# Optimization experiments

Measured on AMD Instinct MI355X. Metric: run time of the kernel, lower is better.

## Reference

```python
import jax, jax.numpy as jnp
import numpy as np

EMB = 1024
HEADS = 16
HEAD_DIM = EMB // HEADS
EPS = 1e-5


def gelu_tanh(x):
    c = jnp.sqrt(jnp.asarray(2.0 / jnp.pi, x.dtype))
    return 0.5 * x * (1.0 + jnp.tanh(c * (x + 0.044715 * x ** 3)))


def layernorm(x, scale, shift):
    mean = jnp.mean(x, axis=-1, keepdims=True)
    var = jnp.mean((x - mean) ** 2, axis=-1, keepdims=True)
    return scale * (x - mean) / jnp.sqrt(var + EPS) + shift


def setup_inputs() -> dict:
    key = jax.random.key(0)
    ks = jax.random.split(key, 12)
    s = 0.02
    return {
        "x": jax.random.normal(ks[0], (2, 2048, EMB), dtype=jnp.float32),
        "Wq": jax.random.normal(ks[1], (EMB, EMB), dtype=jnp.float32) * s,
        "Wk": jax.random.normal(ks[2], (EMB, EMB), dtype=jnp.float32) * s,
        "Wv": jax.random.normal(ks[3], (EMB, EMB), dtype=jnp.float32) * s,
        "Wo": jax.random.normal(ks[4], (EMB, EMB), dtype=jnp.float32) * s,
        "bo": jnp.zeros((EMB,), dtype=jnp.float32),
        "W1": jax.random.normal(ks[5], (EMB, 4 * EMB), dtype=jnp.float32) * s,
        "b1": jnp.zeros((4 * EMB,), dtype=jnp.float32),
        "W2": jax.random.normal(ks[6], (4 * EMB, EMB), dtype=jnp.float32) * s,
        "b2": jnp.zeros((EMB,), dtype=jnp.float32),
        "ln1_scale": jnp.ones((EMB,), dtype=jnp.float32),
        "ln1_shift": jnp.zeros((EMB,), dtype=jnp.float32),
        "ln2_scale": jnp.ones((EMB,), dtype=jnp.float32),
        "ln2_shift": jnp.zeros((EMB,), dtype=jnp.float32),
    }


def reference(x, Wq, Wk, Wv, Wo, bo, W1, b1, W2, b2,
              ln1_scale, ln1_shift, ln2_scale, ln2_shift):
    b, n, d = x.shape
    # --- attention sublayer (pre-LN) ---
    h = layernorm(x, ln1_scale, ln1_shift)
    q = (h @ Wq).reshape(b, n, HEADS, HEAD_DIM).transpose(0, 2, 1, 3)  # [b,h,n,hd]
    k = (h @ Wk).reshape(b, n, HEADS, HEAD_DIM).transpose(0, 2, 1, 3)
    v = (h @ Wv).reshape(b, n, HEADS, HEAD_DIM).transpose(0, 2, 1, 3)
    scores = jnp.einsum('bhqd,bhkd->bhqk', q, k)  # [b,h,n,n]
    causal = jnp.tril(jnp.ones((n, n), dtype=bool))  # True = keep
    scores = jnp.where(causal, scores, -jnp.inf)
    weights = jax.nn.softmax(scores / np.sqrt(HEAD_DIM), axis=-1)
    ctx = jnp.einsum('bhqk,bhkd->bqhd', weights, v).reshape(b, n, d)
    attn_out = ctx @ Wo + bo
    x = x + attn_out
    # --- FFN sublayer (pre-LN) ---
    h = layernorm(x, ln2_scale, ln2_shift)
    h = gelu_tanh(h @ W1 + b1) @ W2 + b2
    return x + h
```

## Files before the change

kernel.cpp:

```cpp
#include <hip/hip_runtime.h>
#include <hip/hip_bf16.h>


using bf16 = __hip_bfloat16;
using bf16x8 = __attribute__((ext_vector_type(8))) short;
using f32x4 = __attribute__((ext_vector_type(4))) float;

#define MFMA16(a, b, c) __builtin_amdgcn_mfma_f32_16x16x32_bf16((a), (b), (c), 0, 0, 0)

enum { EPI_BF16 = 0, EPI_BIAS_RES_F32 = 1, EPI_GELU_BF16 = 2 };

__device__ __forceinline__ float cvt_f(float x) { return x; }
__device__ __forceinline__ float cvt_f(bf16 x) { return __bfloat162float(x); }

__device__ __forceinline__ float gelu_f(float x) {
  float z = 0.7978845608028654f * (x + 0.044715f * x * x * x);
  z = fminf(fmaxf(z, -15.f), 15.f);
  float e = __expf(2.f * z);
  return 0.5f * x * (1.f + (e - 1.f) / (e + 1.f));
}

__device__ __forceinline__ void stage16(const bf16* g, bf16* lds_base, int lane) {
#if defined(__has_builtin) && __has_builtin(__builtin_amdgcn_global_load_lds)
  __builtin_amdgcn_global_load_lds(
      (__attribute__((address_space(1))) void*)(void*)g,
      (__attribute__((address_space(3))) void*)lds_base, 16, 0, 0);
#else
  *(int4*)(lds_base + lane * 8) = *(const int4*)g;
#endif
}

template <typename T>
__global__ __launch_bounds__(256) void transpose_bf16_k(
    const T* __restrict__ src, bf16* __restrict__ dst, int sld, int dld) {
  __shared__ float tile[32][33];
  const int tx = threadIdx.x & 31, ty = threadIdx.x >> 5;
  const size_t r0 = (size_t)blockIdx.y * 32, c0 = (size_t)blockIdx.x * 32;
#pragma unroll
  for (int i = 0; i < 32; i += 8)
    tile[ty + i][tx] = cvt_f(src[(r0 + ty + i) * sld + c0 + tx]);
  __syncthreads();
#pragma unroll
  for (int i = 0; i < 32; i += 8)
    dst[(c0 + ty + i) * dld + r0 + tx] = __float2bfloat16(tile[tx][ty + i]);
}

__global__ __launch_bounds__(256) void ln_fwd_k(
    const float* __restrict__ x, const float* __restrict__ gam,
    const float* __restrict__ bet, bf16* __restrict__ out) {
  const int row = blockIdx.x;
  const float4 v = ((const float4*)(x + (size_t)row * 1024))[threadIdx.x];
  float s = v.x + v.y + v.z + v.w;
  float sq = v.x * v.x + v.y * v.y + v.z * v.z + v.w * v.w;
#pragma unroll
  for (int off = 32; off; off >>= 1) {
    s += __shfl_down(s, off);
    sq += __shfl_down(sq, off);
  }
  __shared__ float rs[4], rq[4];
  const int w = threadIdx.x >> 6, lane = threadIdx.x & 63;
  if (lane == 0) { rs[w] = s; rq[w] = sq; }
  __syncthreads();
  s = rs[0] + rs[1] + rs[2] + rs[3];
  sq = rq[0] + rq[1] + rq[2] + rq[3];
  const float mean = s * (1.f / 1024.f);
  const float var = sq * (1.f / 1024.f) - mean * mean;
  const float rstd = rsqrtf(var + 1e-5f);
  const float4 g4 = ((const float4*)gam)[threadIdx.x];
  const float4 b4 = ((const float4*)bet)[threadIdx.x];
  short4 pk;
  bf16* hp = (bf16*)&pk;
  hp[0] = __float2bfloat16((v.x - mean) * rstd * g4.x + b4.x);
  hp[1] = __float2bfloat16((v.y - mean) * rstd * g4.y + b4.y);
  hp[2] = __float2bfloat16((v.z - mean) * rstd * g4.z + b4.z);
  hp[3] = __float2bfloat16((v.w - mean) * rstd * g4.w + b4.w);
  ((short4*)(out + (size_t)row * 1024))[threadIdx.x] = pk;
}

template <int EPI>
__global__ __launch_bounds__(256) void gemm_bt_k(
    const bf16* __restrict__ A, const bf16* __restrict__ BT,
    void* __restrict__ Cout, const float* __restrict__ bias,
    const float* __restrict__ res, int M, int N, int K) {
  __shared__ bf16 As[128 * 64];
  __shared__ bf16 Bs[128 * 64];
  const int tid = threadIdx.x;
  const int w = tid >> 6, lane = tid & 63;
  const int wr = w >> 1, wc = w & 1;
  const int lr = lane & 15, lk = lane >> 4;
  const size_t rowTile = (size_t)blockIdx.y * 128;
  const size_t colTile = (size_t)blockIdx.x * 128;

  const bf16* Ag = A + rowTile * K;
  const bf16* Bg = BT + colTile * K;
  const int srow = lane >> 3;
  const int scol = (lane & 7) * 8;

  const f32x4 z4 = {0.f, 0.f, 0.f, 0.f};
  f32x4 acc[4][4];
#pragma unroll
  for (int i = 0; i < 4; ++i)
#pragma unroll
    for (int j = 0; j < 4; ++j) acc[i][j] = z4;

  for (int kb = 0; kb < K; kb += 64) {
#pragma unroll
    for (int i = 0; i < 4; ++i) {
      const int r = w * 32 + i * 8;
      stage16(Ag + (size_t)(r + srow) * K + kb + scol, &As[r * 64], lane);
      stage16(Bg + (size_t)(r + srow) * K + kb + scol, &Bs[r * 64], lane);
    }
    __syncthreads();
#pragma unroll
    for (int kk = 0; kk < 2; ++kk) {
      bf16x8 af[4], bg[4];
#pragma unroll
      for (int mi = 0; mi < 4; ++mi)
        af[mi] = *(const bf16x8*)&As[(wr * 64 + mi * 16 + lr) * 64 + kk * 32 + lk * 8];
#pragma unroll
      for (int ni = 0; ni < 4; ++ni)
        bg[ni] = *(const bf16x8*)&Bs[(wc * 64 + ni * 16 + lr) * 64 + kk * 32 + lk * 8];
#pragma unroll
      for (int mi = 0; mi < 4; ++mi)
#pragma unroll
        for (int ni = 0; ni < 4; ++ni)
          acc[mi][ni] = MFMA16(af[mi], bg[ni], acc[mi][ni]);
    }
    __syncthreads();
  }

  const size_t baseRow = rowTile + wr * 64;
  const size_t baseCol = colTile + wc * 64;
#pragma unroll
  for (int mi = 0; mi < 4; ++mi)
#pragma unroll
    for (int ni = 0; ni < 4; ++ni) {
      const size_t col = baseCol + ni * 16 + lr;
#pragma unroll
      for (int r = 0; r < 4; ++r) {
        const size_t row = baseRow + mi * 16 + lk * 4 + r;
        const size_t idx = row * (size_t)N + col;
        const float v = acc[mi][ni][r];
        if constexpr (EPI == EPI_BF16) {
          ((bf16*)Cout)[idx] = __float2bfloat16(v);
        } else if constexpr (EPI == EPI_BIAS_RES_F32) {
          ((float*)Cout)[idx] = v + bias[col] + res[idx];
        } else {
          ((bf16*)Cout)[idx] = __float2bfloat16(gelu_f(v + bias[col]));
        }
      }
    }
}

__global__ __launch_bounds__(256) void attn_fwd_k(
    const bf16* __restrict__ QKV, const bf16* __restrict__ VT,
    bf16* __restrict__ ctx) {
  const int qb = blockIdx.x, head = blockIdx.y, batch = blockIdx.z;
  const int tid = threadIdx.x;
  const int w = tid >> 6, lane = tid & 63;
  const int lr = lane & 15, lk = lane >> 4;
  const int qrow_w = qb * 64 + w * 16;

  __shared__ bf16 Ks[64 * 64];
  __shared__ bf16 Vs[64 * 64];
  __shared__ bf16 Ps[4][16 * 64];

  bf16x8 aq0, aq1;
  {
    const bf16* qp = QKV + (size_t)(batch * 2048 + qrow_w + lr) * 3072 + head * 64 + lk * 8;
    aq0 = *(const bf16x8*)qp;
    aq1 = *(const bf16x8*)(qp + 32);
  }
  const f32x4 z4 = {0.f, 0.f, 0.f, 0.f};
  float m0[4], l0[4];
  f32x4 co[4];
#pragma unroll
  for (int r = 0; r < 4; ++r) { m0[r] = -1e30f; l0[r] = 0.f; }
#pragma unroll
  for (int nd = 0; nd < 4; ++nd) co[nd] = z4;

  const bf16* kbase_p = QKV + (size_t)(batch * 2048) * 3072 + 1024 + head * 64;
  const bf16* vbase_p = VT + (size_t)(head * 64) * 4096 + batch * 2048;
  const int srow = tid >> 3;
  const int scol = (tid & 7) * 8;

  for (int kb = 0; kb <= qb; ++kb) {
    const int kb64 = kb * 64;
    *(int4*)&Ks[srow * 64 + scol]        = *(const int4*)&kbase_p[(size_t)(kb64 + srow) * 3072 + scol];
    *(int4*)&Ks[(srow + 32) * 64 + scol] = *(const int4*)&kbase_p[(size_t)(kb64 + srow + 32) * 3072 + scol];
    *(int4*)&Vs[srow * 64 + scol]        = *(const int4*)&vbase_p[(size_t)srow * 4096 + kb64 + scol];
    *(int4*)&Vs[(srow + 32) * 64 + scol] = *(const int4*)&vbase_p[(size_t)(srow + 32) * 4096 + kb64 + scol];
    __syncthreads();

    f32x4 sv[4];
#pragma unroll
    for (int ni = 0; ni < 4; ++ni) {
      const bf16x8 bk0 = *(const bf16x8*)&Ks[(ni * 16 + lr) * 64 + lk * 8];
      const bf16x8 bk1 = *(const bf16x8*)&Ks[(ni * 16 + lr) * 64 + 32 + lk * 8];
      f32x4 z = z4;
      z = MFMA16(aq0, bk0, z);
      z = MFMA16(aq1, bk1, z);
      sv[ni] = z;
    }
    const bool diag = (kb == qb);
#pragma unroll
    for (int ni = 0; ni < 4; ++ni)
#pragma unroll
      for (int r = 0; r < 4; ++r) {
        float v = sv[ni][r] * 0.125f;
        if (diag && (kb64 + ni * 16 + lr > qrow_w + lk * 4 + r)) v = -1e30f;
        sv[ni][r] = v;
      }
    float fac[4];
#pragma unroll
    for (int r = 0; r < 4; ++r) {
      float mx = fmaxf(fmaxf(sv[0][r], sv[1][r]), fmaxf(sv[2][r], sv[3][r]));
      mx = fmaxf(mx, __shfl_xor(mx, 1));
      mx = fmaxf(mx, __shfl_xor(mx, 2));
      mx = fmaxf(mx, __shfl_xor(mx, 4));
      mx = fmaxf(mx, __shfl_xor(mx, 8));
      const float mn = fmaxf(m0[r], mx);
      fac[r] = __expf(m0[r] - mn);
      m0[r] = mn;
    }
#pragma unroll
    for (int ni = 0; ni < 4; ++ni)
#pragma unroll
      for (int r = 0; r < 4; ++r) sv[ni][r] = __expf(sv[ni][r] - m0[r]);
#pragma unroll
    for (int r = 0; r < 4; ++r) {
      float ps = sv[0][r] + sv[1][r] + sv[2][r] + sv[3][r];
      ps += __shfl_xor(ps, 1);
      ps += __shfl_xor(ps, 2);
      ps += __shfl_xor(ps, 4);
      ps += __shfl_xor(ps, 8);
      l0[r] = l0[r] * fac[r] + ps;
    }
#pragma unroll
    for (int ni = 0; ni < 4; ++ni)
#pragma unroll
      for (int r = 0; r < 4; ++r)
        Ps[w][(lk * 4 + r) * 64 + ni * 16 + lr] = __float2bfloat16(sv[ni][r]);
#pragma unroll
    for (int nd = 0; nd < 4; ++nd)
#pragma unroll
      for (int r = 0; r < 4; ++r) co[nd][r] *= fac[r];
#pragma unroll
    for (int kk = 0; kk < 2; ++kk) {
      const bf16x8 ap = *(const bf16x8*)&Ps[w][lr * 64 + kk * 32 + lk * 8];
#pragma unroll
      for (int nd = 0; nd < 4; ++nd) {
        const bf16x8 bv = *(const bf16x8*)&Vs[(nd * 16 + lr) * 64 + kk * 32 + lk * 8];
        co[nd] = MFMA16(ap, bv, co[nd]);
      }
    }
    __syncthreads();
  }
#pragma unroll
  for (int nd = 0; nd < 4; ++nd)
#pragma unroll
    for (int r = 0; r < 4; ++r) {
      const float v = co[nd][r] / l0[r];
      const size_t row = (size_t)(batch * 2048 + qrow_w + lk * 4 + r);
      ctx[row * 1024 + head * 64 + nd * 16 + lr] = __float2bfloat16(v);
    }
}

extern "C" void kernel_launch(void* const* d_in, const int* in_sizes, int n_in,
                              void* d_out, int out_size, void* d_ws, size_t ws_size,
                              hipStream_t stream) {
  const float* x    = (const float*)d_in[0];
  const float* Wq   = (const float*)d_in[1];
  const float* Wk   = (const float*)d_in[2];
  const float* Wv   = (const float*)d_in[3];
  const float* Wo   = (const float*)d_in[4];
  const float* bo   = (const float*)d_in[5];
  const float* W1   = (const float*)d_in[6];
  const float* b1   = (const float*)d_in[7];
  const float* W2   = (const float*)d_in[8];
  const float* b2   = (const float*)d_in[9];
  const float* ln1s = (const float*)d_in[10];
  const float* ln1b = (const float*)d_in[11];
  const float* ln2s = (const float*)d_in[12];
  const float* ln2b = (const float*)d_in[13];
  float* out = (float*)d_out;

  char* ws = (char*)d_ws;
  const size_t MB = 1ull << 20;
  bf16* WqkvT = (bf16*)(ws + 0);
  bf16* WoT   = (bf16*)(ws + 6 * MB);
  bf16* W1T   = (bf16*)(ws + 8 * MB);
  bf16* W2T   = (bf16*)(ws + 16 * MB);
  bf16* h1    = (bf16*)(ws + 24 * MB);
  bf16* QKV   = (bf16*)(ws + 32 * MB);
  bf16* VT    = (bf16*)(ws + 56 * MB);
  bf16* f1    = (bf16*)(ws + 32 * MB);
  bf16* ctx   = (bf16*)(ws + 64 * MB);

  const dim3 T(256);

  transpose_bf16_k<float><<<dim3(32, 32), T, 0, stream>>>(Wq, WqkvT, 1024, 1024);
  transpose_bf16_k<float><<<dim3(32, 32), T, 0, stream>>>(Wk, WqkvT + 1024 * 1024, 1024, 1024);
  transpose_bf16_k<float><<<dim3(32, 32), T, 0, stream>>>(Wv, WqkvT + 2048 * 1024, 1024, 1024);
  transpose_bf16_k<float><<<dim3(32, 32), T, 0, stream>>>(Wo, WoT, 1024, 1024);
  transpose_bf16_k<float><<<dim3(128, 32), T, 0, stream>>>(W1, W1T, 4096, 1024);
  transpose_bf16_k<float><<<dim3(32, 128), T, 0, stream>>>(W2, W2T, 1024, 4096);

  ln_fwd_k<<<4096, T, 0, stream>>>(x, ln1s, ln1b, h1);

  gemm_bt_k<EPI_BF16><<<dim3(24, 32), T, 0, stream>>>(
      h1, WqkvT, QKV, nullptr, nullptr, 4096, 3072, 1024);

  transpose_bf16_k<bf16><<<dim3(32, 128), T, 0, stream>>>(QKV + 2048, VT, 3072, 4096);

  attn_fwd_k<<<dim3(32, 16, 2), T, 0, stream>>>(QKV, VT, ctx);

  gemm_bt_k<EPI_BIAS_RES_F32><<<dim3(8, 32), T, 0, stream>>>(
      ctx, WoT, out, bo, x, 4096, 1024, 1024);

  ln_fwd_k<<<4096, T, 0, stream>>>(out, ln2s, ln2b, h1);

  gemm_bt_k<EPI_GELU_BF16><<<dim3(32, 32), T, 0, stream>>>(
      h1, W1T, f1, b1, nullptr, 4096, 4096, 1024);

  gemm_bt_k<EPI_BIAS_RES_F32><<<dim3(8, 32), T, 0, stream>>>(
      f1, W2T, out, b2, out, 4096, 1024, 4096);
}
```

Before: 507.7 us.

## Pair causal query blocks in attention, swizzle LDS, and narrow N-tile for small GEMMs

Each attention block now handles query block qp together with its mirror 31-qp. This balances causal work across blocks and lets the two share each K/V tile load. K, V and P tiles in LDS use an XOR swizzle to avoid bank conflicts on MFMA operand reads. The GEMM is templated on BN, and the two N=1024 GEMMs use 128x64 tiles to double the block count (256 to 512) for better CU occupancy. In exchange, attention uses more registers for two accumulator sets and launches half as many blocks.

After: 424.3 us. 16.4% less time.

```diff
diff --git a/kernel.cpp b/kernel.cpp
--- a/kernel.cpp
+++ b/kernel.cpp
@@ -77,19 +77,21 @@
   ((short4*)(out + (size_t)row * 1024))[threadIdx.x] = pk;
 }
 
-template <int EPI>
+template <int EPI, int BN>
 __global__ __launch_bounds__(256) void gemm_bt_k(
     const bf16* __restrict__ A, const bf16* __restrict__ BT,
     void* __restrict__ Cout, const float* __restrict__ bias,
     const float* __restrict__ res, int M, int N, int K) {
+  constexpr int WC = BN / 64;
+  constexpr int MI = 2 * WC;
   __shared__ bf16 As[128 * 64];
-  __shared__ bf16 Bs[128 * 64];
+  __shared__ bf16 Bs[BN * 64];
   const int tid = threadIdx.x;
   const int w = tid >> 6, lane = tid & 63;
-  const int wr = w >> 1, wc = w & 1;
+  const int wc = w % WC, wr = w / WC;
   const int lr = lane & 15, lk = lane >> 4;
   const size_t rowTile = (size_t)blockIdx.y * 128;
-  const size_t colTile = (size_t)blockIdx.x * 128;
+  const size_t colTile = (size_t)blockIdx.x * BN;
 
   const bf16* Ag = A + rowTile * K;
   const bf16* Bg = BT + colTile * K;
@@ -97,9 +99,9 @@
   const int scol = (lane & 7) * 8;
 
   const f32x4 z4 = {0.f, 0.f, 0.f, 0.f};
-  f32x4 acc[4][4];
-#pragma unroll
-  for (int i = 0; i < 4; ++i)
+  f32x4 acc[MI][4];
+#pragma unroll
+  for (int i = 0; i < MI; ++i)
 #pragma unroll
     for (int j = 0; j < 4; ++j) acc[i][j] = z4;
 
@@ -108,20 +110,24 @@
     for (int i = 0; i < 4; ++i) {
       const int r = w * 32 + i * 8;
       stage16(Ag + (size_t)(r + srow) * K + kb + scol, &As[r * 64], lane);
+    }
+#pragma unroll
+    for (int i = 0; i < BN / 32; ++i) {
+      const int r = w * (BN / 4) + i * 8;
       stage16(Bg + (size_t)(r + srow) * K + kb + scol, &Bs[r * 64], lane);
     }
     __syncthreads();
 #pragma unroll
     for (int kk = 0; kk < 2; ++kk) {
-      bf16x8 af[4], bg[4];
-#pragma unroll
-      for (int mi = 0; mi < 4; ++mi)
-        af[mi] = *(const bf16x8*)&As[(wr * 64 + mi * 16 + lr) * 64 + kk * 32 + lk * 8];
+      bf16x8 af[MI], bg[4];
+#pragma unroll
+      for (int mi = 0; mi < MI; ++mi)
+        af[mi] = *(const bf16x8*)&As[(wr * (32 * WC) + mi * 16 + lr) * 64 + kk * 32 + lk * 8];
 #pragma unroll
       for (int ni = 0; ni < 4; ++ni)
         bg[ni] = *(const bf16x8*)&Bs[(wc * 64 + ni * 16 + lr) * 64 + kk * 32 + lk * 8];
 #pragma unroll
-      for (int mi = 0; mi < 4; ++mi)
+      for (int mi = 0; mi < MI; ++mi)
 #pragma unroll
         for (int ni = 0; ni < 4; ++ni)
           acc[mi][ni] = MFMA16(af[mi], bg[ni], acc[mi][ni]);
@@ -129,10 +135,10 @@
     __syncthreads();
   }
 
-  const size_t baseRow = rowTile + wr * 64;
+  const size_t baseRow = rowTile + wr * (32 * WC);
   const size_t baseCol = colTile + wc * 64;
 #pragma unroll
-  for (int mi = 0; mi < 4; ++mi)
+  for (int mi = 0; mi < MI; ++mi)
 #pragma unroll
     for (int ni = 0; ni < 4; ++ni) {
       const size_t col = baseCol + ni * 16 + lr;
@@ -155,54 +161,50 @@
 __global__ __launch_bounds__(256) void attn_fwd_k(
     const bf16* __restrict__ QKV, const bf16* __restrict__ VT,
     bf16* __restrict__ ctx) {
-  const int qb = blockIdx.x, head = blockIdx.y, batch = blockIdx.z;
+  const int qp = blockIdx.x, head = blockIdx.y, batch = blockIdx.z;
   const int tid = threadIdx.x;
   const int w = tid >> 6, lane = tid & 63;
   const int lr = lane & 15, lk = lane >> 4;
-  const int qrow_w = qb * 64 + w * 16;
+  const int qbA = qp, qbB = 31 - qp;
+  const int qrowA = qbA * 64 + w * 16;
+  const int qrowB = qbB * 64 + w * 16;
 
   __shared__ bf16 Ks[64 * 64];
   __shared__ bf16 Vs[64 * 64];
   __shared__ bf16 Ps[4][16 * 64];
 
-  bf16x8 aq0, aq1;
-  {
-    const bf16* qp = QKV + (size_t)(batch * 2048 + qrow_w + lr) * 3072 + head * 64 + lk * 8;
-    aq0 = *(const bf16x8*)qp;
-    aq1 = *(const bf16x8*)(qp + 32);
-  }
+  const bf16* qpa = QKV + (size_t)(batch * 2048 + qrowA + lr) * 3072 + head * 64 + lk * 8;
+  const bf16* qpb = QKV + (size_t)(batch * 2048 + qrowB + lr) * 3072 + head * 64 + lk * 8;
+  const bf16x8 aqA0 = *(const bf16x8*)qpa, aqA1 = *(const bf16x8*)(qpa + 32);
+  const bf16x8 aqB0 = *(const bf16x8*)qpb, aqB1 = *(const bf16x8*)(qpb + 32);
+
   const f32x4 z4 = {0.f, 0.f, 0.f, 0.f};
-  float m0[4], l0[4];
-  f32x4 co[4];
-#pragma unroll
-  for (int r = 0; r < 4; ++r) { m0[r] = -1e30f; l0[r] = 0.f; }
-#pragma unroll
-  for (int nd = 0; nd < 4; ++nd) co[nd] = z4;
-
-  const bf16* kbase_p = QKV + (size_t)(batch * 2048) * 3072 + 1024 + head * 64;
-  const bf16* vbase_p = VT + (size_t)(head * 64) * 4096 + batch * 2048;
+  float mA[4], lA[4], mB[4], lB[4];
+  f32x4 coA[4], coB[4];
+#pragma unroll
+  for (int r = 0; r < 4; ++r) { mA[r] = mB[r] = -1e30f; lA[r] = lB[r] = 0.f; }
+#pragma unroll
+  for (int nd = 0; nd < 4; ++nd) { coA[nd] = z4; coB[nd] = z4; }
+
+  const bf16* kbase = QKV + (size_t)(batch * 2048) * 3072 + 1024 + head * 64;
+  const bf16* vbase = VT + (size_t)(head * 64) * 4096 + batch * 2048;
   const int srow = tid >> 3;
   const int scol = (tid & 7) * 8;
-
-  for (int kb = 0; kb <= qb; ++kb) {
-    const int kb64 = kb * 64;
-    *(int4*)&Ks[srow * 64 + scol]        = *(const int4*)&kbase_p[(size_t)(kb64 + srow) * 3072 + scol];
-    *(int4*)&Ks[(srow + 32) * 64 + scol] = *(const int4*)&kbase_p[(size_t)(kb64 + srow + 32) * 3072 + scol];
-    *(int4*)&Vs[srow * 64 + scol]        = *(const int4*)&vbase_p[(size_t)srow * 4096 + kb64 + scol];
-    *(int4*)&Vs[(srow + 32) * 64 + scol] = *(const int4*)&vbase_p[(size_t)(srow + 32) * 4096 + kb64 + scol];
-    __syncthreads();
-
+  const int swoff = ((tid & 7) ^ (srow & 7)) * 8;
+  const int eQ = (lk ^ (lr & 7)) << 3;
+
+  auto attn_step = [&](int qrow_w, bool diag, int kb64, float* m0, float* l0,
+                       f32x4* co, bf16x8 aq0, bf16x8 aq1) {
     f32x4 sv[4];
 #pragma unroll
     for (int ni = 0; ni < 4; ++ni) {
-      const bf16x8 bk0 = *(const bf16x8*)&Ks[(ni * 16 + lr) * 64 + lk * 8];
-      const bf16x8 bk1 = *(const bf16x8*)&Ks[(ni * 16 + lr) * 64 + 32 + lk * 8];
+      const bf16x8 bk0 = *(const bf16x8*)&Ks[(ni * 16 + lr) * 64 + eQ];
+      const bf16x8 bk1 = *(const bf16x8*)&Ks[(ni * 16 + lr) * 64 + (eQ ^ 32)];
       f32x4 z = z4;
       z = MFMA16(aq0, bk0, z);
       z = MFMA16(aq1, bk1, z);
       sv[ni] = z;
     }
-    const bool diag = (kb == qb);
 #pragma unroll
     for (int ni = 0; ni < 4; ++ni)
 #pragma unroll
@@ -239,30 +241,49 @@
 #pragma unroll
     for (int ni = 0; ni < 4; ++ni)
 #pragma unroll
-      for (int r = 0; r < 4; ++r)
-        Ps[w][(lk * 4 + r) * 64 + ni * 16 + lr] = __float2bfloat16(sv[ni][r]);
+      for (int r = 0; r < 4; ++r) {
+        const int prow = lk * 4 + r;
+        const int pcol = (((ni * 2 + (lr >> 3)) ^ (prow & 7)) << 3) + (lr & 7);
+        Ps[w][prow * 64 + pcol] = __float2bfloat16(sv[ni][r]);
+      }
 #pragma unroll
     for (int nd = 0; nd < 4; ++nd)
 #pragma unroll
       for (int r = 0; r < 4; ++r) co[nd][r] *= fac[r];
 #pragma unroll
     for (int kk = 0; kk < 2; ++kk) {
-      const bf16x8 ap = *(const bf16x8*)&Ps[w][lr * 64 + kk * 32 + lk * 8];
+      const int ep = kk ? (eQ ^ 32) : eQ;
+      const bf16x8 ap = *(const bf16x8*)&Ps[w][lr * 64 + ep];
 #pragma unroll
       for (int nd = 0; nd < 4; ++nd) {
-        const bf16x8 bv = *(const bf16x8*)&Vs[(nd * 16 + lr) * 64 + kk * 32 + lk * 8];
+        const bf16x8 bv = *(const bf16x8*)&Vs[(nd * 16 + lr) * 64 + ep];
         co[nd] = MFMA16(ap, bv, co[nd]);
       }
     }
+  };
+
+  for (int kb = 0; kb <= qbB; ++kb) {
+    const int kb64 = kb * 64;
+    *(int4*)&Ks[srow * 64 + swoff]        = *(const int4*)&kbase[(size_t)(kb64 + srow) * 3072 + scol];
+    *(int4*)&Ks[(srow + 32) * 64 + swoff] = *(const int4*)&kbase[(size_t)(kb64 + srow + 32) * 3072 + scol];
+    *(int4*)&Vs[srow * 64 + swoff]        = *(const int4*)&vbase[(size_t)srow * 4096 + kb64 + scol];
+    *(int4*)&Vs[(srow + 32) * 64 + swoff] = *(const int4*)&vbase[(size_t)(srow + 32) * 4096 + kb64 + scol];
+    __syncthreads();
+
+    attn_step(qrowB, kb == qbB, kb64, mB, lB, coB, aqB0, aqB1);
+    if (kb <= qbA)
+      attn_step(qrowA, kb == qbA, kb64, mA, lA, coA, aqA0, aqA1);
     __syncthreads();
   }
+
 #pragma unroll
   for (int nd = 0; nd < 4; ++nd)
 #pragma unroll
     for (int r = 0; r < 4; ++r) {
-      const float v = co[nd][r] / l0[r];
-      const size_t row = (size_t)(batch * 2048 + qrow_w + lk * 4 + r);
-      ctx[row * 1024 + head * 64 + nd * 16 + lr] = __float2bfloat16(v);
+      const size_t rowA = (size_t)(batch * 2048 + qrowA + lk * 4 + r);
+      ctx[rowA * 1024 + head * 64 + nd * 16 + lr] = __float2bfloat16(coA[nd][r] / lA[r]);
+      const size_t rowB = (size_t)(batch * 2048 + qrowB + lk * 4 + r);
+      ctx[rowB * 1024 + head * 64 + nd * 16 + lr] = __float2bfloat16(coB[nd][r] / lB[r]);
     }
 }
 
@@ -308,21 +329,21 @@
 
   ln_fwd_k<<<4096, T, 0, stream>>>(x, ln1s, ln1b, h1);
 
-  gemm_bt_k<EPI_BF16><<<dim3(24, 32), T, 0, stream>>>(
+  gemm_bt_k<EPI_BF16, 128><<<dim3(24, 32), T, 0, stream>>>(
       h1, WqkvT, QKV, nullptr, nullptr, 4096, 3072, 1024);
 
   transpose_bf16_k<bf16><<<dim3(32, 128), T, 0, stream>>>(QKV + 2048, VT, 3072, 4096);
 
-  attn_fwd_k<<<dim3(32, 16, 2), T, 0, stream>>>(QKV, VT, ctx);
-
-  gemm_bt_k<EPI_BIAS_RES_F32><<<dim3(8, 32), T, 0, stream>>>(
+  attn_fwd_k<<<dim3(16, 16, 2), T, 0, stream>>>(QKV, VT, ctx);
+
+  gemm_bt_k<EPI_BIAS_RES_F32, 64><<<dim3(16, 32), T, 0, stream>>>(
       ctx, WoT, out, bo, x, 4096, 1024, 1024);
 
   ln_fwd_k<<<4096, T, 0, stream>>>(out, ln2s, ln2b, h1);
 
-  gemm_bt_k<EPI_GELU_BF16><<<dim3(32, 32), T, 0, stream>>>(
+  gemm_bt_k<EPI_GELU_BF16, 128><<<dim3(32, 32), T, 0, stream>>>(
       h1, W1T, f1, b1, nullptr, 4096, 4096, 1024);
 
-  gemm_bt_k<EPI_BIAS_RES_F32><<<dim3(8, 32), T, 0, stream>>>(
+  gemm_bt_k<EPI_BIAS_RES_F32, 64><<<dim3(16, 32), T, 0, stream>>>(
       f1, W2T, out, b2, out, 4096, 1024, 4096);
 }
```
